# Kernel optimization log

Hardware: AMD Instinct MI355X
Metric: run time of the kernel (lower is better)

Reference implementation:

```python
import jax, jax.numpy as jnp
import numpy as np

N_NODES = 100000
N_EDGES = 1600000
IN_DIM = 256
HIDDEN = 128
N_CLASSES = 40


def gcn_conv(x, W, b, src, dst, n_nodes):
    """torch_geometric GCNConv: transform -> add self-loops -> sym-normalized sum-aggregate -> +bias."""
    h = x @ W  # [N, out]
    loop = jnp.arange(n_nodes, dtype=src.dtype)
    src2 = jnp.concatenate([src, loop])
    dst2 = jnp.concatenate([dst, loop])
    # degree with self-loops (edge weight 1)
    deg = jax.ops.segment_sum(jnp.ones_like(dst2, dtype=h.dtype), dst2, num_segments=n_nodes)
    dinv = jnp.where(deg > 0, jax.lax.rsqrt(deg), 0.0)
    norm = dinv[src2] * dinv[dst2]  # [E+N]
    msg = h[src2] * norm[:, None]   # [E+N, out] gather + scale
    out = jax.ops.segment_sum(msg, dst2, num_segments=n_nodes)
    return out + b


def setup_inputs() -> dict:
    key = jax.random.key(0)
    k1, k2, k3, k4 = jax.random.split(key, 4)
    x = jax.random.normal(k1, (N_NODES, IN_DIM), dtype=jnp.float32)
    edge_index = jax.random.randint(k2, (2, N_EDGES), 0, N_NODES, dtype=jnp.int64)
    W1 = jax.random.normal(k3, (IN_DIM, HIDDEN), dtype=jnp.float32) * (1.0 / np.sqrt(IN_DIM))
    b1 = jnp.zeros((HIDDEN,), dtype=jnp.float32)
    W2 = jax.random.normal(k4, (HIDDEN, N_CLASSES), dtype=jnp.float32) * (1.0 / np.sqrt(HIDDEN))
    b2 = jnp.zeros((N_CLASSES,), dtype=jnp.float32)
    return {"x": x, "edge_index": edge_index, "W1": W1, "b1": b1, "W2": W2, "b2": b2}


def reference(x, edge_index, W1, b1, W2, b2):
    src, dst = edge_index[0], edge_index[1]
    h = gcn_conv(x, W1, b1, src, dst, N_NODES)
    h = jax.nn.relu(h)
    # dropout p=0.5 is identity in eval mode
    out = gcn_conv(h, W2, b2, src, dst, N_NODES)
    return out
```

## Files before the change

kernel.cpp:

```cpp
#include <hip/hip_runtime.h>
#include <hip/hip_bf16.h>
#include <hip/hip_fp16.h>

#define N_NODES 100000
#define N_EDGES 1600000
#define IN_DIM 256
#define HIDDEN 128
#define NCLS 40
#define NCLS_PAD 48

#define N_BUCKETS 256
#define NPB 391
#define BCAP 8192
#define EPT 16
#define BIN_WG 4096
#define BIN_BLOCKS 391
#define GEMM1_BLOCKS 782

typedef __attribute__((ext_vector_type(8))) _Float16 half8;
typedef __attribute__((ext_vector_type(4))) _Float16 half4f;
typedef __attribute__((ext_vector_type(4))) float floatx4;


__global__ __launch_bounds__(256) void k_prep(const float* __restrict__ W1, __half* __restrict__ W1T,
                                              const float* __restrict__ W2, __half* __restrict__ W2T,
                                              int* __restrict__ bfill) {
    const int t = threadIdx.x;
    if (blockIdx.x < 128) {
        int i = blockIdx.x * 256 + t;
        int k = i >> 7, n = i & 127;
        W1T[n * IN_DIM + k] = __float2half_rn(W1[i]);
    } else if (blockIdx.x == 128) {
        for (int i = t; i < NCLS_PAD * HIDDEN; i += 256) {
            int n = i >> 7, k = i & 127;
            W2T[n * HIDDEN + k] = (n < NCLS) ? __float2half_rn(W2[k * NCLS + n]) : __float2half_rn(0.f);
        }
    } else {
        bfill[t] = 0;
    }
}


__global__ __launch_bounds__(256) void k_binmm(const int* __restrict__ src, const int* __restrict__ dst,
                                               int* __restrict__ bfill,
                                               unsigned long long* __restrict__ bpair,
                                               const float* __restrict__ X,
                                               const __half* __restrict__ W1T,
                                               __half* __restrict__ H1s) {
    __shared__ __align__(16) char smraw[39936];
    const int t = threadIdx.x;

    if (blockIdx.x < BIN_BLOCKS) {
        int* hist   = (int*)smraw;
        int* bstart = hist + 256;
        int* gbase  = bstart + 256;
        unsigned long long* stage = (unsigned long long*)(smraw + 3072);
        unsigned char* bid = (unsigned char*)(smraw + 3072 + 32768);
        hist[t] = 0;
        __syncthreads();
        const long e0 = (long)blockIdx.x * BIN_WG;
        const int n_valid = (int)min((long)BIN_WG, (long)N_EDGES - e0);
        int msrc[EPT], mdst[EPT], moff[EPT];
        #pragma unroll
        for (int i = 0; i < EPT; i++) {
            long e = e0 + t + i * 256;
            if (e < N_EDGES) {
                msrc[i] = src[e];
                mdst[i] = dst[e];
                moff[i] = atomicAdd(&hist[mdst[i] / NPB], 1);
            } else {
                mdst[i] = -1;
            }
        }
        __syncthreads();
        if (t < 64) {
            int carry = 0;
            #pragma unroll
            for (int c = 0; c < 4; c++) {
                int idx = c * 64 + t;
                int hv = hist[idx];
                int s = hv;
                #pragma unroll
                for (int d2 = 1; d2 < 64; d2 <<= 1) {
                    int u = __shfl_up(s, d2, 64);
                    if (t >= d2) s += u;
                }
                bstart[idx] = carry + (s - hv);
                carry += __shfl(s, 63, 64);
            }
        }
        __syncthreads();
        int h = hist[t];
        gbase[t] = (h > 0) ? atomicAdd(&bfill[t], h) : 0;
        #pragma unroll
        for (int i = 0; i < EPT; i++) {
            if (mdst[i] >= 0) {
                int b = mdst[i] / NPB;
                int pos = bstart[b] + moff[i];
                stage[pos] = ((unsigned long long)(unsigned)mdst[i] << 32) | (unsigned)msrc[i];
                bid[pos] = (unsigned char)b;
            }
        }
        __syncthreads();
        for (int i = t; i < n_valid; i += 256) {
            int b = bid[i];
            int dest = gbase[b] + (i - bstart[b]);
            bpair[(long)b * BCAP + dest] = stage[i];
        }
        return;
    }

    _Float16 (*Asm)[72] = (_Float16(*)[72])smraw;
    _Float16 (*Bsm)[72] = (_Float16(*)[72])(smraw + 128 * 72 * 2);
    const int wave = t >> 6;
    const int lane = t & 63;
    const int m16  = lane & 15;
    const int kq   = lane >> 4;
    const int row0 = (blockIdx.x - BIN_BLOCKS) * 128;

    floatx4 acc[2][8];
    #pragma unroll
    for (int mt = 0; mt < 2; mt++)
        #pragma unroll
        for (int i = 0; i < 8; i++) acc[mt][i] = (floatx4)0.f;

    for (int kc = 0; kc < 4; kc++) {
        #pragma unroll
        for (int it = 0; it < 4; it++) {
            int u = t + it * 256;
            int r = u >> 3, j = u & 7;
            int gr = row0 + r;
            float4 x0 = make_float4(0.f, 0.f, 0.f, 0.f), x1 = x0;
            if (gr < N_NODES) {
                const float* p = &X[(long)gr * IN_DIM + kc * 64 + j * 8];
                x0 = *(const float4*)p;
                x1 = *(const float4*)(p + 4);
            }
            half8 hh;
            hh[0] = (_Float16)x0.x; hh[1] = (_Float16)x0.y; hh[2] = (_Float16)x0.z; hh[3] = (_Float16)x0.w;
            hh[4] = (_Float16)x1.x; hh[5] = (_Float16)x1.y; hh[6] = (_Float16)x1.z; hh[7] = (_Float16)x1.w;
            *(half8*)&Asm[r][j * 8] = hh;
        }
        #pragma unroll
        for (int it = 0; it < 4; it++) {
            int u = t + it * 256;
            int n = u >> 3, j = u & 7;
            float4 w = *(const float4*)&W1T[n * IN_DIM + kc * 64 + j * 8];
            *(float4*)&Bsm[n][j * 8] = w;
        }
        __syncthreads();
        #pragma unroll
        for (int ks = 0; ks < 2; ks++) {
            half8 a0 = *(const half8*)&Asm[wave * 32 + m16][ks * 32 + kq * 8];
            half8 a1 = *(const half8*)&Asm[wave * 32 + 16 + m16][ks * 32 + kq * 8];
            #pragma unroll
            for (int nt = 0; nt < 8; nt++) {
                half8 b = *(const half8*)&Bsm[nt * 16 + m16][ks * 32 + kq * 8];
                acc[0][nt] = __builtin_amdgcn_mfma_f32_16x16x32_f16(a0, b, acc[0][nt], 0, 0, 0);
                acc[1][nt] = __builtin_amdgcn_mfma_f32_16x16x32_f16(a1, b, acc[1][nt], 0, 0, 0);
            }
        }
        __syncthreads();
    }
    #pragma unroll
    for (int mt = 0; mt < 2; mt++) {
        const int gr0 = row0 + wave * 32 + mt * 16 + kq * 4;
        #pragma unroll
        for (int nt = 0; nt < 8; nt++) {
            int c = nt * 16 + m16;
            #pragma unroll
            for (int r = 0; r < 4; r++) {
                if (gr0 + r < N_NODES)
                    H1s[(long)(gr0 + r) * HIDDEN + c] = __float2half_rn(acc[mt][nt][r]);
            }
        }
    }
}


__global__ __launch_bounds__(256) void k_build(const int* __restrict__ bfill,
                                               const unsigned long long* __restrict__ bpair,
                                               int* __restrict__ row_ptr, float* __restrict__ dinv,
                                               int* __restrict__ col, __half* __restrict__ H1s) {
    __shared__ int h[NPB];
    __shared__ int pfx[NPB];
    __shared__ float sdinv[NPB];
    __shared__ int sred[4];
    const int b  = blockIdx.x;
    const int nb = b * NPB;
    const int nn = min(NPB, N_NODES - nb);
    const int t  = threadIdx.x;
    int v = (t < b) ? bfill[t] : 0;
    #pragma unroll
    for (int dl = 32; dl > 0; dl >>= 1) v += __shfl_down(v, dl, 64);
    if ((t & 63) == 0) sred[t >> 6] = v;
    for (int i = t; i < NPB; i += 256) h[i] = 0;
    __syncthreads();
    const int base_b = sred[0] + sred[1] + sred[2] + sred[3];
    const int n = bfill[b];
    for (int i = t; i < n; i += 256) {
        int dd = (int)(bpair[(long)b * BCAP + i] >> 32);
        atomicAdd(&h[dd - nb], 1);
    }
    __syncthreads();
    if (t < 64) {
        int carry = 0;
        #pragma unroll
        for (int c = 0; c < (NPB + 63) / 64; c++) {
            int idx = c * 64 + t;
            int hv = (idx < nn) ? h[idx] : 0;
            int s = hv;
            #pragma unroll
            for (int d2 = 1; d2 < 64; d2 <<= 1) {
                int u = __shfl_up(s, d2, 64);
                if (t >= d2) s += u;
            }
            if (idx < nn) {
                int ex = base_b + carry + (s - hv);
                pfx[idx] = ex;
                row_ptr[nb + idx] = ex;
                float dv = rsqrtf((float)(hv + 1));
                dinv[nb + idx] = dv;
                sdinv[idx] = dv;
            }
            carry += __shfl(s, 63, 64);
        }
    }
    __syncthreads();
    for (int i = t; i < nn; i += 256) h[i] = 0;
    __syncthreads();
    for (int i = t; i < n; i += 256) {
        unsigned long long p = bpair[(long)b * BCAP + i];
        int dd = (int)(p >> 32);
        int ss = (int)(p & 0xFFFFFFFFu);
        int pos = pfx[dd - nb] + atomicAdd(&h[dd - nb], 1);
        col[pos] = ss;
    }
    __half2* Hp = (__half2*)H1s;
    for (int i = t; i < nn * 64; i += 256) {
        int r = i >> 6, o = i & 63;
        float dv = sdinv[r];
        float2 f = __half22float2(Hp[(long)(nb + r) * 64 + o]);
        Hp[(long)(nb + r) * 64 + o] = __halves2half2(__float2half_rn(f.x * dv), __float2half_rn(f.y * dv));
    }
    if (b == 0 && t == 0) row_ptr[N_NODES] = N_EDGES;
}


__global__ __launch_bounds__(256) void k_agg1g2(const __half* __restrict__ H1s,
                                                const int* __restrict__ row_ptr,
                                                const int* __restrict__ col,
                                                const float* __restrict__ dinv,
                                                const float* __restrict__ b1,
                                                const __half* __restrict__ W2T,
                                                __half* __restrict__ H2s) {
    __shared__ __align__(16) _Float16 rows[16][136];
    const int wave = threadIdx.x >> 6;
    const int lane = threadIdx.x & 63;
    const __half2* base = (const __half2*)H1s;
    const float2 bb = ((const float2*)b1)[lane];
    const int d00 = blockIdx.x * 16 + wave * 4;

    #pragma unroll
    for (int i = 0; i < 4; i++) {
        const int d = d00 + i;
        int e0 = row_ptr[d], e1 = row_ptr[d + 1];
        float ax = 0.f, ay = 0.f;
        int e = e0;
        for (; e + 3 < e1; e += 4) {
            int s0 = col[e], s1 = col[e + 1], s2 = col[e + 2], s3 = col[e + 3];
            float2 f0 = __half22float2(base[(long)s0 * 64 + lane]);
            float2 f1 = __half22float2(base[(long)s1 * 64 + lane]);
            float2 f2 = __half22float2(base[(long)s2 * 64 + lane]);
            float2 f3 = __half22float2(base[(long)s3 * 64 + lane]);
            ax += f0.x + f1.x + f2.x + f3.x;
            ay += f0.y + f1.y + f2.y + f3.y;
        }
        for (; e < e1; e++) {
            float2 f = __half22float2(base[(long)col[e] * 64 + lane]);
            ax += f.x; ay += f.y;
        }
        float2 fs = __half22float2(base[(long)d * 64 + lane]);
        ax += fs.x; ay += fs.y;
        const float dd = dinv[d];
        float ox = fmaxf(dd * ax + bb.x, 0.f) * dd;
        float oy = fmaxf(dd * ay + bb.y, 0.f) * dd;
        *(__half2*)&rows[wave * 4 + i][lane * 2] =
            __halves2half2(__float2half_rn(ox), __float2half_rn(oy));
    }
    __syncthreads();

    if (wave < 3) {
        const int m16 = lane & 15;
        const int kq  = lane >> 4;
        floatx4 acc = (floatx4)0.f;
        #pragma unroll
        for (int ks = 0; ks < 4; ks++) {
            half8 a = *(const half8*)&rows[m16][ks * 32 + kq * 8];
            half8 b = *(const half8*)&W2T[(wave * 16 + m16) * HIDDEN + ks * 32 + kq * 8];
            acc = __builtin_amdgcn_mfma_f32_16x16x32_f16(a, b, acc, 0, 0, 0);
        }
        const int c = wave * 16 + m16;
        if (c < NCLS) {
            const int gr0 = blockIdx.x * 16 + kq * 4;
            #pragma unroll
            for (int r = 0; r < 4; r++)
                H2s[(long)(gr0 + r) * NCLS + c] = __float2half_rn(acc[r]);
        }
    }
}


__global__ __launch_bounds__(256) void k_agg2(const __half* __restrict__ H2s,
                                              const int* __restrict__ row_ptr,
                                              const int* __restrict__ col,
                                              const float* __restrict__ dinv,
                                              const float* __restrict__ b2,
                                              float* __restrict__ out) {
    const int wave = threadIdx.x >> 6;
    const int lane = threadIdx.x & 63;
    const int g = lane / 10;
    const int f = lane - g * 10;
    const int d = blockIdx.x * 24 + wave * 6 + g;
    const bool act = (g < 6) && (d < N_NODES);
    int e0 = 0, e1 = 0;
    if (act) { e0 = row_ptr[d]; e1 = row_ptr[d + 1]; }
    const half4f* base4 = (const half4f*)H2s;
    float s0 = 0.f, s1 = 0.f, s2 = 0.f, s3 = 0.f;
    int e = e0;
    while (__any(e < e1)) {
        if (e < e1) {
            half4f v = base4[(long)col[e] * 10 + f];
            s0 += (float)v[0]; s1 += (float)v[1]; s2 += (float)v[2]; s3 += (float)v[3];
        }
        if (e + 1 < e1) {
            half4f v = base4[(long)col[e + 1] * 10 + f];
            s0 += (float)v[0]; s1 += (float)v[1]; s2 += (float)v[2]; s3 += (float)v[3];
        }
        e += 2;
    }
    if (act) {
        half4f v = base4[(long)d * 10 + f];
        s0 += (float)v[0]; s1 += (float)v[1]; s2 += (float)v[2]; s3 += (float)v[3];
        float dd = dinv[d];
        float4 bbv = ((const float4*)b2)[f];
        float4 o = make_float4(dd * s0 + bbv.x, dd * s1 + bbv.y, dd * s2 + bbv.z, dd * s3 + bbv.w);
        ((float4*)out)[(long)d * 10 + f] = o;
    }
}


extern "C" void kernel_launch(void* const* d_in, const int* in_sizes, int n_in,
                              void* d_out, int out_size, void* d_ws, size_t ws_size,
                              hipStream_t stream) {
    const float* x  = (const float*)d_in[0];
    const int*   ei = (const int*)d_in[1];
    const float* W1 = (const float*)d_in[2];
    const float* b1 = (const float*)d_in[3];
    const float* W2 = (const float*)d_in[4];
    const float* b2 = (const float*)d_in[5];
    const int* srcE = ei;
    const int* dstE = ei + N_EDGES;

    int*   row_ptr = (int*)d_ws;
    int*   bfill   = row_ptr + 100032;
    int*   col     = bfill + 256;
    float* dinv    = (float*)(col + N_EDGES);
    __half* H1s    = (__half*)(dinv + 100032);
    __half* H2s    = H1s + (long)N_NODES * HIDDEN;
    __half* W1T    = H2s + (long)N_NODES * NCLS;
    __half* W2T    = W1T + IN_DIM * HIDDEN;
    unsigned long long* bpair = (unsigned long long*)(W2T + NCLS_PAD * HIDDEN);

    k_prep   <<<130, 256, 0, stream>>>(W1, W1T, W2, W2T, bfill);
    k_binmm  <<<BIN_BLOCKS + GEMM1_BLOCKS, 256, 0, stream>>>(srcE, dstE, bfill, bpair, x, W1T, H1s);
    k_build  <<<N_BUCKETS, 256, 0, stream>>>(bfill, bpair, row_ptr, dinv, col, H1s);
    k_agg1g2 <<<N_NODES / 16, 256, 0, stream>>>(H1s, row_ptr, col, dinv, b1, W2T, H2s);
    k_agg2   <<<(N_NODES + 23) / 24, 256, 0, stream>>>(H2s, row_ptr, col, dinv, b2, (float*)d_out);
}
```

Before: 359.4 us.

## Move source dinv scaling into layer-1 gather, split edges across half-waves

Drops the pass in k_build that rescaled every H1 row by its source dinv, which cost a full read and write of H1. Layer-1 aggregation now loads dinv[col] for each edge and applies it while gathering. Each wave's two 32-lane halves take alternate edges with 8-byte half4 loads and combine via a shuffle. The layer-2 gather loop is unrolled to 4 edges. The trade-off is an extra random dinv load per edge and a less balanced, predicated inner loop.

```diff
diff --git a/kernel.cpp b/kernel.cpp
--- a/kernel.cpp
+++ b/kernel.cpp
@@ -181,10 +181,9 @@
 __global__ __launch_bounds__(256) void k_build(const int* __restrict__ bfill,
                                                const unsigned long long* __restrict__ bpair,
                                                int* __restrict__ row_ptr, float* __restrict__ dinv,
-                                               int* __restrict__ col, __half* __restrict__ H1s) {
+                                               int* __restrict__ col) {
     __shared__ int h[NPB];
     __shared__ int pfx[NPB];
-    __shared__ float sdinv[NPB];
     __shared__ int sred[4];
     const int b  = blockIdx.x;
     const int nb = b * NPB;
@@ -219,9 +218,7 @@
                 int ex = base_b + carry + (s - hv);
                 pfx[idx] = ex;
                 row_ptr[nb + idx] = ex;
-                float dv = rsqrtf((float)(hv + 1));
-                dinv[nb + idx] = dv;
-                sdinv[idx] = dv;
+                dinv[nb + idx] = rsqrtf((float)(hv + 1));
             }
             carry += __shfl(s, 63, 64);
         }
@@ -235,13 +232,6 @@
         int ss = (int)(p & 0xFFFFFFFFu);
         int pos = pfx[dd - nb] + atomicAdd(&h[dd - nb], 1);
         col[pos] = ss;
-    }
-    __half2* Hp = (__half2*)H1s;
-    for (int i = t; i < nn * 64; i += 256) {
-        int r = i >> 6, o = i & 63;
-        float dv = sdinv[r];
-        float2 f = __half22float2(Hp[(long)(nb + r) * 64 + o]);
-        Hp[(long)(nb + r) * 64 + o] = __halves2half2(__float2half_rn(f.x * dv), __float2half_rn(f.y * dv));
     }
     if (b == 0 && t == 0) row_ptr[N_NODES] = N_EDGES;
 }
@@ -257,36 +247,54 @@
     __shared__ __align__(16) _Float16 rows[16][136];
     const int wave = threadIdx.x >> 6;
     const int lane = threadIdx.x & 63;
-    const __half2* base = (const __half2*)H1s;
-    const float2 bb = ((const float2*)b1)[lane];
+    const int f    = lane & 31;
+    const int hf   = lane >> 5;
+    const half4f* base4 = (const half4f*)H1s;
+    const float4 bb = ((const float4*)b1)[f];
     const int d00 = blockIdx.x * 16 + wave * 4;
 
     #pragma unroll
     for (int i = 0; i < 4; i++) {
-        const int d = d00 + i;
-        int e0 = row_ptr[d], e1 = row_ptr[d + 1];
-        float ax = 0.f, ay = 0.f;
-        int e = e0;
-        for (; e + 3 < e1; e += 4) {
-            int s0 = col[e], s1 = col[e + 1], s2 = col[e + 2], s3 = col[e + 3];
-            float2 f0 = __half22float2(base[(long)s0 * 64 + lane]);
-            float2 f1 = __half22float2(base[(long)s1 * 64 + lane]);
-            float2 f2 = __half22float2(base[(long)s2 * 64 + lane]);
-            float2 f3 = __half22float2(base[(long)s3 * 64 + lane]);
-            ax += f0.x + f1.x + f2.x + f3.x;
-            ay += f0.y + f1.y + f2.y + f3.y;
-        }
-        for (; e < e1; e++) {
-            float2 f = __half22float2(base[(long)col[e] * 64 + lane]);
-            ax += f.x; ay += f.y;
-        }
-        float2 fs = __half22float2(base[(long)d * 64 + lane]);
-        ax += fs.x; ay += fs.y;
+        const int d  = d00 + i;
+        const int e1 = row_ptr[d + 1];
+        int e = row_ptr[d] + hf;
         const float dd = dinv[d];
-        float ox = fmaxf(dd * ax + bb.x, 0.f) * dd;
-        float oy = fmaxf(dd * ay + bb.y, 0.f) * dd;
-        *(__half2*)&rows[wave * 4 + i][lane * 2] =
-            __halves2half2(__float2half_rn(ox), __float2half_rn(oy));
+        const half4f sv = base4[(long)d * 32 + f];
+        float a0 = 0.f, a1 = 0.f, a2 = 0.f, a3 = 0.f;
+        while (__any(e < e1)) {
+            #pragma unroll
+            for (int u = 0; u < 4; u++) {
+                const int ee = e + u * 2;
+                if (ee < e1) {
+                    const int s = col[ee];
+                    const float dv = dinv[s];
+                    const half4f vv = base4[(long)s * 32 + f];
+                    a0 += dv * (float)vv[0];
+                    a1 += dv * (float)vv[1];
+                    a2 += dv * (float)vv[2];
+                    a3 += dv * (float)vv[3];
+                }
+            }
+            e += 8;
+        }
+        a0 += __shfl_xor(a0, 32, 64);
+        a1 += __shfl_xor(a1, 32, 64);
+        a2 += __shfl_xor(a2, 32, 64);
+        a3 += __shfl_xor(a3, 32, 64);
+        a0 += dd * (float)sv[0];
+        a1 += dd * (float)sv[1];
+        a2 += dd * (float)sv[2];
+        a3 += dd * (float)sv[3];
+        const float o0 = fmaxf(dd * a0 + bb.x, 0.f) * dd;
+        const float o1 = fmaxf(dd * a1 + bb.y, 0.f) * dd;
+        const float o2 = fmaxf(dd * a2 + bb.z, 0.f) * dd;
+        const float o3 = fmaxf(dd * a3 + bb.w, 0.f) * dd;
+        if (hf == 0) {
+            half4f hv;
+            hv[0] = (_Float16)o0; hv[1] = (_Float16)o1;
+            hv[2] = (_Float16)o2; hv[3] = (_Float16)o3;
+            *(half4f*)&rows[wave * 4 + i][f * 4] = hv;
+        }
     }
     __syncthreads();
 
@@ -329,15 +337,14 @@
     float s0 = 0.f, s1 = 0.f, s2 = 0.f, s3 = 0.f;
     int e = e0;
     while (__any(e < e1)) {
-        if (e < e1) {
-            half4f v = base4[(long)col[e] * 10 + f];
-            s0 += (float)v[0]; s1 += (float)v[1]; s2 += (float)v[2]; s3 += (float)v[3];
-        }
-        if (e + 1 < e1) {
-            half4f v = base4[(long)col[e + 1] * 10 + f];
-            s0 += (float)v[0]; s1 += (float)v[1]; s2 += (float)v[2]; s3 += (float)v[3];
-        }
-        e += 2;
+        #pragma unroll
+        for (int u = 0; u < 4; u++) {
+            if (e + u < e1) {
+                half4f v = base4[(long)col[e + u] * 10 + f];
+                s0 += (float)v[0]; s1 += (float)v[1]; s2 += (float)v[2]; s3 += (float)v[3];
+            }
+        }
+        e += 4;
     }
     if (act) {
         half4f v = base4[(long)d * 10 + f];
@@ -374,7 +381,7 @@
 
     k_prep   <<<130, 256, 0, stream>>>(W1, W1T, W2, W2T, bfill);
     k_binmm  <<<BIN_BLOCKS + GEMM1_BLOCKS, 256, 0, stream>>>(srcE, dstE, bfill, bpair, x, W1T, H1s);
-    k_build  <<<N_BUCKETS, 256, 0, stream>>>(bfill, bpair, row_ptr, dinv, col, H1s);
+    k_build  <<<N_BUCKETS, 256, 0, stream>>>(bfill, bpair, row_ptr, dinv, col);
     k_agg1g2 <<<N_NODES / 16, 256, 0, stream>>>(H1s, row_ptr, col, dinv, b1, W2T, H2s);
     k_agg2   <<<(N_NODES + 23) / 24, 256, 0, stream>>>(H2s, row_ptr, col, dinv, b2, (float*)d_out);
 }
```

Result: slower. 369.3 us (+2.8%).

## Precompute degrees with atomics and fold dinv scaling into GEMM epilogue

Applied to the files above, without the earlier changes.

Node degrees are now computed up front by a separate atomic-histogram kernel plus an rsqrt kernel, instead of inside the CSR build. That lets the first GEMM epilogue multiply each output row by dinv before the fp16 store. This removes the separate read-modify-write pass over H1 in k_build. The aggregation gather loops are also unrolled further: 8-way in layer 1 with readfirstlane on the row bounds, and 4-way in layer 2. The cost is two extra launches, a second read of dst, and 1.6M global atomics; the degree array reuses the bpair buffer before binning overwrites it.

```diff
diff --git a/kernel.cpp b/kernel.cpp
--- a/kernel.cpp
+++ b/kernel.cpp
@@ -24,7 +24,7 @@
 
 __global__ __launch_bounds__(256) void k_prep(const float* __restrict__ W1, __half* __restrict__ W1T,
                                               const float* __restrict__ W2, __half* __restrict__ W2T,
-                                              int* __restrict__ bfill) {
+                                              int* __restrict__ bfill, int* __restrict__ deg) {
     const int t = threadIdx.x;
     if (blockIdx.x < 128) {
         int i = blockIdx.x * 256 + t;
@@ -35,9 +35,26 @@
             int n = i >> 7, k = i & 127;
             W2T[n * HIDDEN + k] = (n < NCLS) ? __float2half_rn(W2[k * NCLS + n]) : __float2half_rn(0.f);
         }
+    } else if (blockIdx.x == 129) {
+        bfill[t] = 0;
     } else {
-        bfill[t] = 0;
-    }
+        int i = (blockIdx.x - 130) * 256 + t;
+        if (i < N_NODES) deg[i] = 0;
+    }
+}
+
+
+__global__ __launch_bounds__(256) void k_deg(const int* __restrict__ dst, int* __restrict__ deg) {
+    long e = (long)blockIdx.x * 2048 + threadIdx.x;
+    #pragma unroll
+    for (int i = 0; i < 8; i++, e += 256)
+        if (e < N_EDGES) atomicAdd(&deg[dst[e]], 1);
+}
+
+
+__global__ __launch_bounds__(256) void k_dinv(const int* __restrict__ deg, float* __restrict__ dinv) {
+    int i = blockIdx.x * 256 + threadIdx.x;
+    if (i < N_NODES) dinv[i] = rsqrtf((float)(deg[i] + 1));
 }
 
 
@@ -46,6 +63,7 @@
                                                unsigned long long* __restrict__ bpair,
                                                const float* __restrict__ X,
                                                const __half* __restrict__ W1T,
+                                               const float* __restrict__ dinv,
                                                __half* __restrict__ H1s) {
     __shared__ __align__(16) char smraw[39936];
     const int t = threadIdx.x;
@@ -165,13 +183,17 @@
     #pragma unroll
     for (int mt = 0; mt < 2; mt++) {
         const int gr0 = row0 + wave * 32 + mt * 16 + kq * 4;
+        float dv[4];
+        #pragma unroll
+        for (int r = 0; r < 4; r++)
+            dv[r] = (gr0 + r < N_NODES) ? dinv[gr0 + r] : 0.f;
         #pragma unroll
         for (int nt = 0; nt < 8; nt++) {
             int c = nt * 16 + m16;
             #pragma unroll
             for (int r = 0; r < 4; r++) {
                 if (gr0 + r < N_NODES)
-                    H1s[(long)(gr0 + r) * HIDDEN + c] = __float2half_rn(acc[mt][nt][r]);
+                    H1s[(long)(gr0 + r) * HIDDEN + c] = __float2half_rn(acc[mt][nt][r] * dv[r]);
             }
         }
     }
@@ -180,11 +202,10 @@
 
 __global__ __launch_bounds__(256) void k_build(const int* __restrict__ bfill,
                                                const unsigned long long* __restrict__ bpair,
-                                               int* __restrict__ row_ptr, float* __restrict__ dinv,
-                                               int* __restrict__ col, __half* __restrict__ H1s) {
+                                               int* __restrict__ row_ptr,
+                                               int* __restrict__ col) {
     __shared__ int h[NPB];
     __shared__ int pfx[NPB];
-    __shared__ float sdinv[NPB];
     __shared__ int sred[4];
     const int b  = blockIdx.x;
     const int nb = b * NPB;
@@ -219,9 +240,6 @@
                 int ex = base_b + carry + (s - hv);
                 pfx[idx] = ex;
                 row_ptr[nb + idx] = ex;
-                float dv = rsqrtf((float)(hv + 1));
-                dinv[nb + idx] = dv;
-                sdinv[idx] = dv;
             }
             carry += __shfl(s, 63, 64);
         }
@@ -235,13 +253,6 @@
         int ss = (int)(p & 0xFFFFFFFFu);
         int pos = pfx[dd - nb] + atomicAdd(&h[dd - nb], 1);
         col[pos] = ss;
-    }
-    __half2* Hp = (__half2*)H1s;
-    for (int i = t; i < nn * 64; i += 256) {
-        int r = i >> 6, o = i & 63;
-        float dv = sdinv[r];
-        float2 f = __half22float2(Hp[(long)(nb + r) * 64 + o]);
-        Hp[(long)(nb + r) * 64 + o] = __halves2half2(__float2half_rn(f.x * dv), __float2half_rn(f.y * dv));
     }
     if (b == 0 && t == 0) row_ptr[N_NODES] = N_EDGES;
 }
@@ -264,17 +275,32 @@
     #pragma unroll
     for (int i = 0; i < 4; i++) {
         const int d = d00 + i;
-        int e0 = row_ptr[d], e1 = row_ptr[d + 1];
+        const int e0 = __builtin_amdgcn_readfirstlane(row_ptr[d]);
+        const int e1 = __builtin_amdgcn_readfirstlane(row_ptr[d + 1]);
         float ax = 0.f, ay = 0.f;
         int e = e0;
+        for (; e + 7 < e1; e += 8) {
+            int s0 = col[e],     s1 = col[e + 1], s2 = col[e + 2], s3 = col[e + 3];
+            int s4 = col[e + 4], s5 = col[e + 5], s6 = col[e + 6], s7 = col[e + 7];
+            float2 f0 = __half22float2(base[(long)s0 * 64 + lane]);
+            float2 f1 = __half22float2(base[(long)s1 * 64 + lane]);
+            float2 f2 = __half22float2(base[(long)s2 * 64 + lane]);
+            float2 f3 = __half22float2(base[(long)s3 * 64 + lane]);
+            float2 f4 = __half22float2(base[(long)s4 * 64 + lane]);
+            float2 f5 = __half22float2(base[(long)s5 * 64 + lane]);
+            float2 f6 = __half22float2(base[(long)s6 * 64 + lane]);
+            float2 f7 = __half22float2(base[(long)s7 * 64 + lane]);
+            ax += ((f0.x + f1.x) + (f2.x + f3.x)) + ((f4.x + f5.x) + (f6.x + f7.x));
+            ay += ((f0.y + f1.y) + (f2.y + f3.y)) + ((f4.y + f5.y) + (f6.y + f7.y));
+        }
         for (; e + 3 < e1; e += 4) {
             int s0 = col[e], s1 = col[e + 1], s2 = col[e + 2], s3 = col[e + 3];
             float2 f0 = __half22float2(base[(long)s0 * 64 + lane]);
             float2 f1 = __half22float2(base[(long)s1 * 64 + lane]);
             float2 f2 = __half22float2(base[(long)s2 * 64 + lane]);
             float2 f3 = __half22float2(base[(long)s3 * 64 + lane]);
-            ax += f0.x + f1.x + f2.x + f3.x;
-            ay += f0.y + f1.y + f2.y + f3.y;
+            ax += (f0.x + f1.x) + (f2.x + f3.x);
+            ay += (f0.y + f1.y) + (f2.y + f3.y);
         }
         for (; e < e1; e++) {
             float2 f = __half22float2(base[(long)col[e] * 64 + lane]);
@@ -329,15 +355,14 @@
     float s0 = 0.f, s1 = 0.f, s2 = 0.f, s3 = 0.f;
     int e = e0;
     while (__any(e < e1)) {
-        if (e < e1) {
-            half4f v = base4[(long)col[e] * 10 + f];
-            s0 += (float)v[0]; s1 += (float)v[1]; s2 += (float)v[2]; s3 += (float)v[3];
-        }
-        if (e + 1 < e1) {
-            half4f v = base4[(long)col[e + 1] * 10 + f];
-            s0 += (float)v[0]; s1 += (float)v[1]; s2 += (float)v[2]; s3 += (float)v[3];
-        }
-        e += 2;
+        #pragma unroll
+        for (int u = 0; u < 4; u++) {
+            if (e + u < e1) {
+                half4f v = base4[(long)col[e + u] * 10 + f];
+                s0 += (float)v[0]; s1 += (float)v[1]; s2 += (float)v[2]; s3 += (float)v[3];
+            }
+        }
+        e += 4;
     }
     if (act) {
         half4f v = base4[(long)d * 10 + f];
@@ -371,10 +396,13 @@
     __half* W1T    = H2s + (long)N_NODES * NCLS;
     __half* W2T    = W1T + IN_DIM * HIDDEN;
     unsigned long long* bpair = (unsigned long long*)(W2T + NCLS_PAD * HIDDEN);
-
-    k_prep   <<<130, 256, 0, stream>>>(W1, W1T, W2, W2T, bfill);
-    k_binmm  <<<BIN_BLOCKS + GEMM1_BLOCKS, 256, 0, stream>>>(srcE, dstE, bfill, bpair, x, W1T, H1s);
-    k_build  <<<N_BUCKETS, 256, 0, stream>>>(bfill, bpair, row_ptr, dinv, col, H1s);
+    int*   deg     = (int*)bpair;
+
+    k_prep   <<<521, 256, 0, stream>>>(W1, W1T, W2, W2T, bfill, deg);
+    k_deg    <<<782, 256, 0, stream>>>(dstE, deg);
+    k_dinv   <<<391, 256, 0, stream>>>(deg, dinv);
+    k_binmm  <<<BIN_BLOCKS + GEMM1_BLOCKS, 256, 0, stream>>>(srcE, dstE, bfill, bpair, x, W1T, dinv, H1s);
+    k_build  <<<N_BUCKETS, 256, 0, stream>>>(bfill, bpair, row_ptr, col);
     k_agg1g2 <<<N_NODES / 16, 256, 0, stream>>>(H1s, row_ptr, col, dinv, b1, W2T, H2s);
     k_agg2   <<<(N_NODES + 23) / 24, 256, 0, stream>>>(H2s, row_ptr, col, dinv, b2, (float*)d_out);
 }
```

After: 406.6 us. 13.1% more time.
